# Performance work log

Measured on AMD Instinct MI355X. Metric: run time of the kernel, lower is better.

Reference implementation:

```python
import jax, jax.numpy as jnp
import numpy as np

OUT_FEATURES = 11008
IN_FEATURES = 4096
PACKED_LEN = OUT_FEATURES * IN_FEATURES // 4  # 4 ternary vals per byte, 2 bits each


def setup_inputs() -> dict:
    key = jax.random.key(0)
    k1, k2, k3 = jax.random.split(key, 3)
    x = jax.random.normal(k1, (4, 1024, IN_FEATURES), dtype=jnp.float32)
    packed_weight = jax.random.randint(k2, (PACKED_LEN,), 0, 256, dtype=jnp.int32)
    weight_scale = jax.random.uniform(k3, (1,), dtype=jnp.float32)
    return {"x": x, "packed_weight": packed_weight, "weight_scale": weight_scale}


def _dequantize_weight(packed_weight, weight_scale):
    shifts = jnp.arange(0, 8, 2, dtype=jnp.int32)          # [4]
    q = ((packed_weight[:, None] >> shifts) & 3) - 1        # [P, 4]
    q = q.reshape(OUT_FEATURES, IN_FEATURES).astype(jnp.float32)
    return q * weight_scale.reshape(())                      # dequantize


def reference(x, packed_weight, weight_scale):
    w = _dequantize_weight(packed_weight, weight_scale)      # [out, in]
    # F.linear: y = x @ w.T  (bias=False)
    return jnp.einsum('bsi,oi->bso', x, w)
```

## Files before the change

### kernel.cpp

```cpp
#include <hip/hip_runtime.h>
#include <hip/hip_bf16.h>

#define OUT_F 11008
#define IN_F  4096
#define M_DIM 4096

typedef __attribute__((ext_vector_type(8))) short bf16x8;
typedef __attribute__((ext_vector_type(4))) float f32x4;
typedef __attribute__((ext_vector_type(8))) unsigned short us8;

__device__ __forceinline__ unsigned short f2bf_rne(float f) {
    unsigned u = __builtin_bit_cast(unsigned, f);
    u += 0x7fffu + ((u >> 16) & 1u);
    return (unsigned short)(u >> 16);
}

__global__ void cvt_x_kernel(const float* __restrict__ x,
                             unsigned short* __restrict__ xb) {
    size_t i = ((size_t)blockIdx.x * blockDim.x + threadIdx.x) * 8;
    float4 a = *(const float4*)(x + i);
    float4 b = *(const float4*)(x + i + 4);
    us8 o;
    o[0] = f2bf_rne(a.x); o[1] = f2bf_rne(a.y);
    o[2] = f2bf_rne(a.z); o[3] = f2bf_rne(a.w);
    o[4] = f2bf_rne(b.x); o[5] = f2bf_rne(b.y);
    o[6] = f2bf_rne(b.z); o[7] = f2bf_rne(b.w);
    *(us8*)(xb + i) = o;
}

__global__ void unpack_w_kernel(const int* __restrict__ pw,
                                unsigned short* __restrict__ wb) {
    size_t i = (size_t)blockIdx.x * blockDim.x + threadIdx.x;
    int4 v = ((const int4*)pw)[i];
    const unsigned long long LUT = 0x40003F800000BF80ull;
    us8 o0, o1;
#pragma unroll
    for (int j = 0; j < 4; j++) {
        o0[j]     = (unsigned short)(LUT >> (((v.x >> (2 * j)) & 3) * 16));
        o0[4 + j] = (unsigned short)(LUT >> (((v.y >> (2 * j)) & 3) * 16));
        o1[j]     = (unsigned short)(LUT >> (((v.z >> (2 * j)) & 3) * 16));
        o1[4 + j] = (unsigned short)(LUT >> (((v.w >> (2 * j)) & 3) * 16));
    }
    ((us8*)wb)[i * 2]     = o0;
    ((us8*)wb)[i * 2 + 1] = o1;
}

#define LGKM0() do { asm volatile("s_waitcnt lgkmcnt(0)" ::: "memory"); \
                     __builtin_amdgcn_sched_barrier(0); } while (0)
#define VMCNT(n) do { asm volatile("s_waitcnt vmcnt(" #n ")" ::: "memory"); \
                      __builtin_amdgcn_sched_barrier(0); } while (0)

__global__ __launch_bounds__(512, 2) void gemm_kernel(
    const unsigned short* __restrict__ A,
    const unsigned short* __restrict__ B,
    float* __restrict__ C,
    const float* __restrict__ scale_ptr) {
    constexpr int K  = IN_F;
    constexpr int N  = OUT_F;
    constexpr int NT = K / 64;

    __shared__ unsigned short lds[2][2][2][256][32];

    const int tid  = threadIdx.x;
    const int wave = tid >> 6;
    const int lane = tid & 63;
    const int quad = lane >> 4;
    const int mrow = lane & 15;
    const int sw   = quad ^ ((mrow >> 1) & 3);

    const int srow = lane >> 2;
    const int sseg = (lane & 3) ^ ((lane >> 3) & 3);

    const int lin = blockIdx.x;
    const int xcd = lin & 7;
    const int q   = lin >> 3;
    const int bm  = xcd * 2 + q / 43;
    const int bn  = q % 43;

    const int wm = (wave >> 2) * 128;
    const int wn = (wave & 3) * 64;

    const unsigned short* Ag = A + (size_t)bm * 256 * K;
    const unsigned short* Bg = B + (size_t)bn * 256 * K;

    f32x4 acc[8][4];
#pragma unroll
    for (int i = 0; i < 8; i++)
#pragma unroll
        for (int j = 0; j < 4; j++) acc[i][j] = (f32x4){0.f, 0.f, 0.f, 0.f};

    auto STAGE = [&](int mat, int nb, int h, int kbase) {
#pragma unroll
        for (int c = 0; c < 2; ++c) {
            const int chunk = wave * 2 + c;
            const int grow  = chunk * 16 + srow;
            const unsigned short* src =
                (mat ? Bg : Ag) + (size_t)grow * K + kbase + sseg * 8;
            __builtin_amdgcn_global_load_lds(
                (const __attribute__((address_space(1))) void*)src,
                (__attribute__((address_space(3))) void*)
                    (&lds[nb][mat][h][0][0] + chunk * 512),
                16, 0, 0);
        }
    };

    STAGE(0, 0, 0, 0);
    STAGE(1, 0, 0, 0);
    STAGE(0, 0, 1, 32);
    STAGE(1, 0, 1, 32);
    VMCNT(4);
    __builtin_amdgcn_s_barrier();

    bf16x8 a[8], b0, b1, b2, b3;

#pragma unroll 2
    for (int kt = 0; kt < NT; ++kt) {
        const int  buf  = kt & 1;
        const int  nbuf = buf ^ 1;
        const bool pf   = (kt + 1 < NT);
        const int  kn   = (kt + 1) * 64;

#pragma unroll
        for (int t = 0; t < 8; ++t)
            a[t] = *(const bf16x8*)&lds[buf][0][0][wm + t * 16 + mrow][sw * 8];
        b0 = *(const bf16x8*)&lds[buf][1][0][wn +  0 + mrow][sw * 8];
        b1 = *(const bf16x8*)&lds[buf][1][0][wn + 16 + mrow][sw * 8];
        if (pf) STAGE(0, nbuf, 0, kn);
        __builtin_amdgcn_s_barrier();
        LGKM0();
        __builtin_amdgcn_s_setprio(1);
#pragma unroll
        for (int t = 0; t < 8; ++t) {
            acc[t][0] = __builtin_amdgcn_mfma_f32_16x16x32_bf16(a[t], b0, acc[t][0], 0, 0, 0);
            acc[t][1] = __builtin_amdgcn_mfma_f32_16x16x32_bf16(a[t], b1, acc[t][1], 0, 0, 0);
        }
        __builtin_amdgcn_s_setprio(0);
        __builtin_amdgcn_s_barrier();

        b2 = *(const bf16x8*)&lds[buf][1][0][wn + 32 + mrow][sw * 8];
        b3 = *(const bf16x8*)&lds[buf][1][0][wn + 48 + mrow][sw * 8];
        if (pf) STAGE(1, nbuf, 0, kn);
        __builtin_amdgcn_s_barrier();
        LGKM0();
        __builtin_amdgcn_s_setprio(1);
#pragma unroll
        for (int t = 0; t < 8; ++t) {
            acc[t][2] = __builtin_amdgcn_mfma_f32_16x16x32_bf16(a[t], b2, acc[t][2], 0, 0, 0);
            acc[t][3] = __builtin_amdgcn_mfma_f32_16x16x32_bf16(a[t], b3, acc[t][3], 0, 0, 0);
        }
        __builtin_amdgcn_s_setprio(0);
        if (pf) { VMCNT(4); } else { VMCNT(0); }
        __builtin_amdgcn_s_barrier();

#pragma unroll
        for (int t = 0; t < 8; ++t)
            a[t] = *(const bf16x8*)&lds[buf][0][1][wm + t * 16 + mrow][sw * 8];
        b0 = *(const bf16x8*)&lds[buf][1][1][wn +  0 + mrow][sw * 8];
        b1 = *(const bf16x8*)&lds[buf][1][1][wn + 16 + mrow][sw * 8];
        if (pf) STAGE(0, nbuf, 1, kn + 32);
        __builtin_amdgcn_s_barrier();
        LGKM0();
        __builtin_amdgcn_s_setprio(1);
#pragma unroll
        for (int t = 0; t < 8; ++t) {
            acc[t][0] = __builtin_amdgcn_mfma_f32_16x16x32_bf16(a[t], b0, acc[t][0], 0, 0, 0);
            acc[t][1] = __builtin_amdgcn_mfma_f32_16x16x32_bf16(a[t], b1, acc[t][1], 0, 0, 0);
        }
        __builtin_amdgcn_s_setprio(0);
        __builtin_amdgcn_s_barrier();

        b2 = *(const bf16x8*)&lds[buf][1][1][wn + 32 + mrow][sw * 8];
        b3 = *(const bf16x8*)&lds[buf][1][1][wn + 48 + mrow][sw * 8];
        if (pf) STAGE(1, nbuf, 1, kn + 32);
        __builtin_amdgcn_s_barrier();
        LGKM0();
        __builtin_amdgcn_s_setprio(1);
#pragma unroll
        for (int t = 0; t < 8; ++t) {
            acc[t][2] = __builtin_amdgcn_mfma_f32_16x16x32_bf16(a[t], b2, acc[t][2], 0, 0, 0);
            acc[t][3] = __builtin_amdgcn_mfma_f32_16x16x32_bf16(a[t], b3, acc[t][3], 0, 0, 0);
        }
        __builtin_amdgcn_s_setprio(0);
        if (pf) { VMCNT(4); }
        __builtin_amdgcn_s_barrier();
    }

    const float scale = *scale_ptr;
    float* Cg = C + (size_t)(bm * 256 + wm) * N + bn * 256 + wn;
#pragma unroll
    for (int i = 0; i < 8; ++i) {
#pragma unroll
        for (int j = 0; j < 4; ++j) {
#pragma unroll
            for (int r = 0; r < 4; ++r) {
                const int row = i * 16 + quad * 4 + r;
                const int col = j * 16 + mrow;
                Cg[(size_t)row * N + col] = acc[i][j][r] * scale;
            }
        }
    }
}

extern "C" void kernel_launch(void* const* d_in, const int* in_sizes, int n_in,
                              void* d_out, int out_size, void* d_ws, size_t ws_size,
                              hipStream_t stream) {
    const float* x   = (const float*)d_in[0];
    const int* pw    = (const int*)d_in[1];
    const float* wsc = (const float*)d_in[2];

    float* out = (float*)d_out;

    unsigned short* xb = (unsigned short*)d_ws;
    unsigned short* wb = (unsigned short*)((char*)d_ws + (size_t)M_DIM * IN_F * 2);

    cvt_x_kernel<<<8192, 256, 0, stream>>>(x, xb);

    unpack_w_kernel<<<11008, 256, 0, stream>>>(pw, wb);

    gemm_kernel<<<688, 512, 0, stream>>>(xb, wb, out, wsc);
}
```

Measured before the change: 587.6 us.

## Shrink GEMM M-tile to 128, split K-step to 32, fuse prep kernels

Merges the x-to-bf16 conversion and the ternary weight unpack into one prep launch. The GEMM tile shrinks from 256x256 to 128x256 and the K step from 64 to 32, which cuts per-wave accumulators so 4 blocks per CU can fit. A and B use separately staged buffers with a prefetch two steps ahead for A. The grid doubles, so the GEMM gets more occupancy in exchange for lower per-block reuse of B tiles and more barriers per unit of K.

```diff
diff --git a/kernel.cpp b/kernel.cpp
--- a/kernel.cpp
+++ b/kernel.cpp
@@ -15,34 +15,35 @@
     return (unsigned short)(u >> 16);
 }
 
-__global__ void cvt_x_kernel(const float* __restrict__ x,
-                             unsigned short* __restrict__ xb) {
-    size_t i = ((size_t)blockIdx.x * blockDim.x + threadIdx.x) * 8;
-    float4 a = *(const float4*)(x + i);
-    float4 b = *(const float4*)(x + i + 4);
-    us8 o;
-    o[0] = f2bf_rne(a.x); o[1] = f2bf_rne(a.y);
-    o[2] = f2bf_rne(a.z); o[3] = f2bf_rne(a.w);
-    o[4] = f2bf_rne(b.x); o[5] = f2bf_rne(b.y);
-    o[6] = f2bf_rne(b.z); o[7] = f2bf_rne(b.w);
-    *(us8*)(xb + i) = o;
-}
-
-__global__ void unpack_w_kernel(const int* __restrict__ pw,
-                                unsigned short* __restrict__ wb) {
-    size_t i = (size_t)blockIdx.x * blockDim.x + threadIdx.x;
-    int4 v = ((const int4*)pw)[i];
-    const unsigned long long LUT = 0x40003F800000BF80ull;
-    us8 o0, o1;
+__global__ void prep_kernel(const float* __restrict__ x,
+                            unsigned short* __restrict__ xb,
+                            const int* __restrict__ pw,
+                            unsigned short* __restrict__ wb) {
+    if (blockIdx.x < 8192) {
+        size_t i = ((size_t)blockIdx.x * blockDim.x + threadIdx.x) * 8;
+        float4 a = *(const float4*)(x + i);
+        float4 b = *(const float4*)(x + i + 4);
+        us8 o;
+        o[0] = f2bf_rne(a.x); o[1] = f2bf_rne(a.y);
+        o[2] = f2bf_rne(a.z); o[3] = f2bf_rne(a.w);
+        o[4] = f2bf_rne(b.x); o[5] = f2bf_rne(b.y);
+        o[6] = f2bf_rne(b.z); o[7] = f2bf_rne(b.w);
+        *(us8*)(xb + i) = o;
+    } else {
+        size_t i = ((size_t)(blockIdx.x - 8192)) * blockDim.x + threadIdx.x;
+        int4 v = ((const int4*)pw)[i];
+        const unsigned long long LUT = 0x40003F800000BF80ull;
+        us8 o0, o1;
 #pragma unroll
-    for (int j = 0; j < 4; j++) {
-        o0[j]     = (unsigned short)(LUT >> (((v.x >> (2 * j)) & 3) * 16));
-        o0[4 + j] = (unsigned short)(LUT >> (((v.y >> (2 * j)) & 3) * 16));
-        o1[j]     = (unsigned short)(LUT >> (((v.z >> (2 * j)) & 3) * 16));
-        o1[4 + j] = (unsigned short)(LUT >> (((v.w >> (2 * j)) & 3) * 16));
+        for (int j = 0; j < 4; j++) {
+            o0[j]     = (unsigned short)(LUT >> (((v.x >> (2 * j)) & 3) * 16));
+            o0[4 + j] = (unsigned short)(LUT >> (((v.y >> (2 * j)) & 3) * 16));
+            o1[j]     = (unsigned short)(LUT >> (((v.z >> (2 * j)) & 3) * 16));
+            o1[4 + j] = (unsigned short)(LUT >> (((v.w >> (2 * j)) & 3) * 16));
+        }
+        ((us8*)wb)[i * 2]     = o0;
+        ((us8*)wb)[i * 2 + 1] = o1;
     }
-    ((us8*)wb)[i * 2]     = o0;
-    ((us8*)wb)[i * 2 + 1] = o1;
 }
 
 #define LGKM0() do { asm volatile("s_waitcnt lgkmcnt(0)" ::: "memory"); \
@@ -50,16 +51,17 @@
 #define VMCNT(n) do { asm volatile("s_waitcnt vmcnt(" #n ")" ::: "memory"); \
                       __builtin_amdgcn_sched_barrier(0); } while (0)
 
-__global__ __launch_bounds__(512, 2) void gemm_kernel(
+__global__ __launch_bounds__(512, 4) void gemm_kernel(
     const unsigned short* __restrict__ A,
     const unsigned short* __restrict__ B,
     float* __restrict__ C,
     const float* __restrict__ scale_ptr) {
     constexpr int K  = IN_F;
     constexpr int N  = OUT_F;
-    constexpr int NT = K / 64;
+    constexpr int NT = K / 32;
 
-    __shared__ unsigned short lds[2][2][2][256][32];
+    __shared__ unsigned short sA[2][128][32];
+    __shared__ unsigned short sB[2][256][32];
 
     const int tid  = threadIdx.x;
     const int wave = tid >> 6;
@@ -74,121 +76,94 @@
     const int lin = blockIdx.x;
     const int xcd = lin & 7;
     const int q   = lin >> 3;
-    const int bm  = xcd * 2 + q / 43;
+    const int bm  = xcd * 4 + q / 43;
     const int bn  = q % 43;
 
-    const int wm = (wave >> 2) * 128;
+    const int wm = (wave >> 2) * 64;
     const int wn = (wave & 3) * 64;
 
-    const unsigned short* Ag = A + (size_t)bm * 256 * K;
+    const unsigned short* Ag = A + (size_t)bm * 128 * K;
     const unsigned short* Bg = B + (size_t)bn * 256 * K;
 
-    f32x4 acc[8][4];
+    f32x4 acc[4][4];
 #pragma unroll
-    for (int i = 0; i < 8; i++)
+    for (int i = 0; i < 4; i++)
 #pragma unroll
         for (int j = 0; j < 4; j++) acc[i][j] = (f32x4){0.f, 0.f, 0.f, 0.f};
 
-    auto STAGE = [&](int mat, int nb, int h, int kbase) {
+    auto STAGE_A = [&](int nb, int kb) {
+        const int row = wave * 16 + srow;
+        const unsigned short* src = Ag + (size_t)row * K + kb + sseg * 8;
+        __builtin_amdgcn_global_load_lds(
+            (const __attribute__((address_space(1))) void*)src,
+            (__attribute__((address_space(3))) void*)(&sA[nb][0][0] + wave * 512),
+            16, 0, 0);
+    };
+    auto STAGE_B = [&](int nb, int kb) {
 #pragma unroll
         for (int c = 0; c < 2; ++c) {
             const int chunk = wave * 2 + c;
-            const int grow  = chunk * 16 + srow;
-            const unsigned short* src =
-                (mat ? Bg : Ag) + (size_t)grow * K + kbase + sseg * 8;
+            const int row = chunk * 16 + srow;
+            const unsigned short* src = Bg + (size_t)row * K + kb + sseg * 8;
             __builtin_amdgcn_global_load_lds(
                 (const __attribute__((address_space(1))) void*)src,
-                (__attribute__((address_space(3))) void*)
-                    (&lds[nb][mat][h][0][0] + chunk * 512),
+                (__attribute__((address_space(3))) void*)(&sB[nb][0][0] + chunk * 512),
                 16, 0, 0);
         }
     };
 
-    STAGE(0, 0, 0, 0);
-    STAGE(1, 0, 0, 0);
-    STAGE(0, 0, 1, 32);
-    STAGE(1, 0, 1, 32);
-    VMCNT(4);
+    STAGE_A(0, 0);
+    STAGE_B(0, 0);
+    STAGE_A(1, 32);
+    VMCNT(1);
     __builtin_amdgcn_s_barrier();
 
-    bf16x8 a[8], b0, b1, b2, b3;
+    bf16x8 a[4], b0, b1, b2, b3;
 
 #pragma unroll 2
     for (int kt = 0; kt < NT; ++kt) {
         const int  buf  = kt & 1;
         const int  nbuf = buf ^ 1;
-        const bool pf   = (kt + 1 < NT);
-        const int  kn   = (kt + 1) * 64;
+        const bool pf1  = (kt + 1 < NT);
+        const bool pf2  = (kt + 2 < NT);
 
 #pragma unroll
-        for (int t = 0; t < 8; ++t)
-            a[t] = *(const bf16x8*)&lds[buf][0][0][wm + t * 16 + mrow][sw * 8];
-        b0 = *(const bf16x8*)&lds[buf][1][0][wn +  0 + mrow][sw * 8];
-        b1 = *(const bf16x8*)&lds[buf][1][0][wn + 16 + mrow][sw * 8];
-        if (pf) STAGE(0, nbuf, 0, kn);
+        for (int t = 0; t < 4; ++t)
+            a[t] = *(const bf16x8*)&sA[buf][wm + t * 16 + mrow][sw * 8];
+        b0 = *(const bf16x8*)&sB[buf][wn +  0 + mrow][sw * 8];
+        b1 = *(const bf16x8*)&sB[buf][wn + 16 + mrow][sw * 8];
+        if (pf1) STAGE_B(nbuf, (kt + 1) * 32);
         __builtin_amdgcn_s_barrier();
         LGKM0();
         __builtin_amdgcn_s_setprio(1);
 #pragma unroll
-        for (int t = 0; t < 8; ++t) {
+        for (int t = 0; t < 4; ++t) {
             acc[t][0] = __builtin_amdgcn_mfma_f32_16x16x32_bf16(a[t], b0, acc[t][0], 0, 0, 0);
             acc[t][1] = __builtin_amdgcn_mfma_f32_16x16x32_bf16(a[t], b1, acc[t][1], 0, 0, 0);
         }
         __builtin_amdgcn_s_setprio(0);
         __builtin_amdgcn_s_barrier();
 
-        b2 = *(const bf16x8*)&lds[buf][1][0][wn + 32 + mrow][sw * 8];
-        b3 = *(const bf16x8*)&lds[buf][1][0][wn + 48 + mrow][sw * 8];
-        if (pf) STAGE(1, nbuf, 0, kn);
+        b2 = *(const bf16x8*)&sB[buf][wn + 32 + mrow][sw * 8];
+        b3 = *(const bf16x8*)&sB[buf][wn + 48 + mrow][sw * 8];
+        if (pf2) STAGE_A(buf, (kt + 2) * 32);
         __builtin_amdgcn_s_barrier();
         LGKM0();
         __builtin_amdgcn_s_setprio(1);
 #pragma unroll
-        for (int t = 0; t < 8; ++t) {
+        for (int t = 0; t < 4; ++t) {
             acc[t][2] = __builtin_amdgcn_mfma_f32_16x16x32_bf16(a[t], b2, acc[t][2], 0, 0, 0);
             acc[t][3] = __builtin_amdgcn_mfma_f32_16x16x32_bf16(a[t], b3, acc[t][3], 0, 0, 0);
         }
         __builtin_amdgcn_s_setprio(0);
-        if (pf) { VMCNT(4); } else { VMCNT(0); }
-        __builtin_amdgcn_s_barrier();
-
-#pragma unroll
-        for (int t = 0; t < 8; ++t)
-            a[t] = *(const bf16x8*)&lds[buf][0][1][wm + t * 16 + mrow][sw * 8];
-        b0 = *(const bf16x8*)&lds[buf][1][1][wn +  0 + mrow][sw * 8];
-        b1 = *(const bf16x8*)&lds[buf][1][1][wn + 16 + mrow][sw * 8];
-        if (pf) STAGE(0, nbuf, 1, kn + 32);
-        __builtin_amdgcn_s_barrier();
-        LGKM0();
-        __builtin_amdgcn_s_setprio(1);
-#pragma unroll
-        for (int t = 0; t < 8; ++t) {
-            acc[t][0] = __builtin_amdgcn_mfma_f32_16x16x32_bf16(a[t], b0, acc[t][0], 0, 0, 0);
-            acc[t][1] = __builtin_amdgcn_mfma_f32_16x16x32_bf16(a[t], b1, acc[t][1], 0, 0, 0);
-        }
-        __builtin_amdgcn_s_setprio(0);
-        __builtin_amdgcn_s_barrier();
-
-        b2 = *(const bf16x8*)&lds[buf][1][1][wn + 32 + mrow][sw * 8];
-        b3 = *(const bf16x8*)&lds[buf][1][1][wn + 48 + mrow][sw * 8];
-        if (pf) STAGE(1, nbuf, 1, kn + 32);
-        __builtin_amdgcn_s_barrier();
-        LGKM0();
-        __builtin_amdgcn_s_setprio(1);
-#pragma unroll
-        for (int t = 0; t < 8; ++t) {
-            acc[t][2] = __builtin_amdgcn_mfma_f32_16x16x32_bf16(a[t], b2, acc[t][2], 0, 0, 0);
-            acc[t][3] = __builtin_amdgcn_mfma_f32_16x16x32_bf16(a[t], b3, acc[t][3], 0, 0, 0);
-        }
-        __builtin_amdgcn_s_setprio(0);
-        if (pf) { VMCNT(4); }
+        if (pf2) { VMCNT(1); } else { VMCNT(0); }
         __builtin_amdgcn_s_barrier();
     }
 
     const float scale = *scale_ptr;
-    float* Cg = C + (size_t)(bm * 256 + wm) * N + bn * 256 + wn;
+    float* Cg = C + (size_t)(bm * 128 + wm) * N + bn * 256 + wn;
 #pragma unroll
-    for (int i = 0; i < 8; ++i) {
+    for (int i = 0; i < 4; ++i) {
 #pragma unroll
         for (int j = 0; j < 4; ++j) {
 #pragma unroll
@@ -213,9 +188,7 @@
     unsigned short* xb = (unsigned short*)d_ws;
     unsigned short* wb = (unsigned short*)((char*)d_ws + (size_t)M_DIM * IN_F * 2);
 
-    cvt_x_kernel<<<8192, 256, 0, stream>>>(x, xb);
+    prep_kernel<<<8192 + 11008, 256, 0, stream>>>(x, xb, pw, wb);
 
-    unpack_w_kernel<<<11008, 256, 0, stream>>>(pw, wb);
-
-    gemm_kernel<<<688, 512, 0, stream>>>(xb, wb, out, wsc);
+    gemm_kernel<<<1376, 512, 0, stream>>>(xb, wb, out, wsc);
 }
```

After: 680.5 us. 15.8% more time.
